# Kernel tuning notes

Hardware: AMD Instinct MI355X
Metric: run time of the kernel (lower is better)

Reference implementation:

```python
import jax, jax.numpy as jnp
import numpy as np

DIM = 1024
HEADS = 16
HEAD_DIM = DIM // HEADS
B, N = 8, 1024


def setup_inputs() -> dict:
    key = jax.random.key(0)
    ks = jax.random.split(key, 10)
    s = lambda fan_in: 1.0 / np.sqrt(fan_in)
    return {
        "x": jax.random.normal(ks[0], (B, N, DIM), jnp.float32),
        "pose_angles": jax.random.normal(ks[1], (B, 3), jnp.float32),
        # weights stored (in, out) so y = x @ W + b (equivalent to torch Linear)
        "Wqkv": jax.random.normal(ks[2], (DIM, 3 * DIM), jnp.float32) * s(DIM),
        "bqkv": jnp.zeros((3 * DIM,), jnp.float32),
        "W1": jax.random.normal(ks[3], (3, 64), jnp.float32) * s(3),
        "b1": jnp.zeros((64,), jnp.float32),
        "W2": jax.random.normal(ks[4], (64, 3 * DIM), jnp.float32) * s(64),
        "b2": jnp.zeros((3 * DIM,), jnp.float32),
        "Wproj": jax.random.normal(ks[5], (DIM, DIM), jnp.float32) * s(DIM),
        "bproj": jnp.zeros((DIM,), jnp.float32),
    }


def reference(x, pose_angles, Wqkv, bqkv, W1, b1, W2, b2, Wproj, bproj):
    Bq, Nq, C = x.shape
    H, D = HEADS, HEAD_DIM
    # qkv projection -> [B,N,3,H,D] -> [3,B,H,N,D]
    qkv = (x @ Wqkv + bqkv).reshape(Bq, Nq, 3, H, D).transpose(2, 0, 3, 1, 4)
    q, k, v = qkv[0], qkv[1], qkv[2]
    # pose MLP: 3 -> 64 -> 3*dim, chunked into per-head biases [B,H,1,D]
    pose_emb = jax.nn.relu(pose_angles @ W1 + b1) @ W2 + b2
    pose_q, pose_k, pose_v = jnp.split(pose_emb, 3, axis=1)
    pose_q = pose_q.reshape(Bq, H, 1, D)
    pose_k = pose_k.reshape(Bq, H, 1, D)
    pose_v = pose_v.reshape(Bq, H, 1, D)
    q = q + pose_q
    k = k + pose_k
    v = v + pose_v
    scale = 1.0 / jnp.sqrt(jnp.asarray(D, x.dtype))
    attn = jax.nn.softmax(jnp.einsum("bhnd,bhmd->bhnm", q, k) * scale, axis=-1)
    # dropout is identity in eval mode
    out = jnp.einsum("bhnm,bhmd->bhnd", attn, v)
    out = out.transpose(0, 2, 1, 3).reshape(Bq, Nq, C)
    return out @ Wproj + bproj
```

## Files before the change

### kernel.cpp

```cpp
#include <hip/hip_runtime.h>
#include <stdint.h>

typedef unsigned short u16;
typedef short bf16x8 __attribute__((ext_vector_type(8)));
typedef short bf16x4 __attribute__((ext_vector_type(4)));
typedef float f32x4 __attribute__((ext_vector_type(4)));
typedef u16 u16x4 __attribute__((ext_vector_type(4)));

__device__ __forceinline__ u16 f2bf(float f) {
  union { float f; unsigned int u; } v; v.f = f;
  unsigned int r = v.u + 0x7fffu + ((v.u >> 16) & 1u);
  return (u16)(r >> 16);
}

__device__ __forceinline__ void async16(const void* g, void* l) {
  __builtin_amdgcn_global_load_lds(
      (const __attribute__((address_space(1))) unsigned int*)g,
      (__attribute__((address_space(3))) unsigned int*)l, 16, 0, 0);
}

__device__ __forceinline__ f32x4 mfma16x16(bf16x4 a, bf16x4 b, f32x4 c) {
#if __has_builtin(__builtin_amdgcn_mfma_f32_16x16x16bf16_1k)
  return __builtin_amdgcn_mfma_f32_16x16x16bf16_1k(a, b, c, 0, 0, 0);
#else
  asm volatile("v_mfma_f32_16x16x16_bf16 %0, %1, %2, %0\n\ts_nop 7\n\ts_nop 7"
               : "+v"(c) : "v"(a), "v"(b));
  return c;
#endif
}

__global__ void pose_mlp_kernel(const float* __restrict__ ang, const float* __restrict__ W1,
                                const float* __restrict__ b1, const float* __restrict__ W2,
                                const float* __restrict__ b2, float* __restrict__ pose) {
  __shared__ float hid[8][64];
  int t = threadIdx.x;
  for (int idx = t; idx < 512; idx += 256) {
    int b = idx >> 6, j = idx & 63;
    float a = b1[j];
#pragma unroll
    for (int i = 0; i < 3; ++i) a += ang[b * 3 + i] * W1[i * 64 + j];
    hid[b][j] = fmaxf(a, 0.f);
  }
  __syncthreads();
  int idx = blockIdx.x * 256 + t;
  int b = idx / 3072, c = idx - b * 3072;
  float a = b2[c];
#pragma unroll
  for (int j = 0; j < 64; ++j) a += hid[b][j] * W2[j * 3072 + c];
  pose[idx] = a;
}

__global__ void cast_x_kernel(const float4* __restrict__ x, u16x4* __restrict__ y, int n4) {
  int i = blockIdx.x * blockDim.x + threadIdx.x;
  const int stride = gridDim.x * blockDim.x;
  for (; i < n4; i += stride) {
    float4 v = x[i];
    u16x4 o;
    o[0] = f2bf(v.x); o[1] = f2bf(v.y); o[2] = f2bf(v.z); o[3] = f2bf(v.w);
    y[i] = o;
  }
}

__global__ void transpose_cast_kernel(const float* __restrict__ W, u16* __restrict__ Wt,
                                      int Kdim, int Ncol) {
  __shared__ float tile[64][65];
  const int tx = threadIdx.x, ty = threadIdx.y;
  const int c0 = blockIdx.x * 64, k0 = blockIdx.y * 64;
#pragma unroll
  for (int rr = 0; rr < 16; ++rr) {
    int row = rr * 4 + ty;
    tile[row][tx] = W[(size_t)(k0 + row) * Ncol + c0 + tx];
  }
  __syncthreads();
#pragma unroll
  for (int rr = 0; rr < 16; ++rr) {
    int row = rr * 4 + ty;
    Wt[(size_t)(c0 + row) * Kdim + k0 + tx] = f2bf(tile[tx][row]);
  }
}

template <int EPI>
__global__ void __launch_bounds__(256) gemm_bt_kernel(
    const u16* __restrict__ A, const u16* __restrict__ Bt,
    const float* __restrict__ bias, const float* __restrict__ pose,
    u16* __restrict__ qout, u16* __restrict__ kout, u16* __restrict__ vtout,
    float* __restrict__ cout, int Kdim, int Ncols, int nTilesX) {
  __shared__ u16 ldsA[2][128 * 64];
  __shared__ u16 ldsB[2][128 * 64];
  const int t = threadIdx.x, l = t & 63, w = t >> 6;
  const int g = l >> 4, r16 = l & 15;
  const int wr = w >> 1, wc = w & 1;
  const int xk = r16 & 7;
  const int nwg = gridDim.x, cpx = nwg >> 3;
  const int swz = (blockIdx.x & 7) * cpx + (blockIdx.x >> 3);
  const int n0 = (swz % nTilesX) * 128, m0 = (swz / nTilesX) * 128;
  const u16* Ab = A + (size_t)m0 * Kdim;
  const u16* Bb = Bt + (size_t)n0 * Kdim;

  auto stage = [&](int buf, int kt) {
#pragma unroll
    for (int ii = 0; ii < 4; ++ii) {
      int idx = ii * 256 + t, row = idx >> 3;
      int seg = (idx & 7) ^ (row & 7);
      async16(Ab + (size_t)row * Kdim + kt + seg * 8, &ldsA[buf][(ii * 256 + w * 64) * 8]);
    }
#pragma unroll
    for (int ii = 0; ii < 4; ++ii) {
      int idx = ii * 256 + t, row = idx >> 3;
      int seg = (idx & 7) ^ (row & 7);
      async16(Bb + (size_t)row * Kdim + kt + seg * 8, &ldsB[buf][(ii * 256 + w * 64) * 8]);
    }
  };

  f32x4 acc[4][4] = {};
  const int nIter = Kdim >> 6;
  stage(0, 0);
  asm volatile("s_waitcnt vmcnt(0)" ::: "memory");
  __builtin_amdgcn_s_barrier();
  int cur = 0;
  for (int it = 0; it < nIter; ++it) {
    if (it + 1 < nIter) stage(cur ^ 1, (it + 1) << 6);
#pragma unroll
    for (int ks = 0; ks < 2; ++ks) {
      bf16x8 a[4], bb[4];
#pragma unroll
      for (int i = 0; i < 4; ++i)
        a[i] = *(const bf16x8*)&ldsA[cur][(wr * 64 + i * 16 + r16) * 64 + ((ks * 4 + g) ^ xk) * 8];
#pragma unroll
      for (int j = 0; j < 4; ++j)
        bb[j] = *(const bf16x8*)&ldsB[cur][(wc * 64 + j * 16 + r16) * 64 + ((ks * 4 + g) ^ xk) * 8];
#pragma unroll
      for (int i = 0; i < 4; ++i)
#pragma unroll
        for (int j = 0; j < 4; ++j)
          acc[i][j] = __builtin_amdgcn_mfma_f32_16x16x32_bf16(a[i], bb[j], acc[i][j], 0, 0, 0);
    }
    asm volatile("s_waitcnt vmcnt(0)" ::: "memory");
    __builtin_amdgcn_s_barrier();
    cur ^= 1;
  }
#pragma unroll
  for (int i = 0; i < 4; ++i)
#pragma unroll
    for (int j = 0; j < 4; ++j)
#pragma unroll
      for (int r = 0; r < 4; ++r) {
        int row = m0 + wr * 64 + i * 16 + g * 4 + r;
        int col = n0 + wc * 64 + j * 16 + r16;
        float v = acc[i][j][r] + bias[col];
        if (EPI == 0) {
          int b = row >> 10, n = row & 1023;
          v += pose[b * 3072 + col];
          u16 hv = f2bf(v);
          int three = col >> 10, hh = (col >> 6) & 15, d = col & 63;
          size_t bhh = (size_t)(b * 16 + hh);
          if (three == 0)      qout[(bhh * 1024 + n) * 64 + d] = hv;
          else if (three == 1) kout[(bhh * 1024 + n) * 64 + d] = hv;
          else                 vtout[(bhh * 64 + d) * 1024 + n] = hv;
        } else {
          cout[(size_t)row * Ncols + col] = v;
        }
      }
}

__global__ void __launch_bounds__(256) attn_kernel(
    const u16* __restrict__ Qb, const u16* __restrict__ Kb,
    const u16* __restrict__ Vtb, u16* __restrict__ aout) {
  __shared__ u16 ldsK[64][72];
  __shared__ u16 ldsV[64][72];
  const int t = threadIdx.x, l = t & 63, w = t >> 6;
  const int g = l >> 4, r16 = l & 15;
  const int bh = blockIdx.x >> 4, qt = blockIdx.x & 15;
  const int b = bh >> 4, h = bh & 15;
  const int q0 = qt * 64 + w * 16;
  const u16* Qp = Qb + ((size_t)bh * 1024 + q0 + r16) * 64;
  bf16x8 qreg0 = *(const bf16x8*)(Qp + g * 8);
  bf16x8 qreg1 = *(const bf16x8*)(Qp + 32 + g * 8);
  const u16* Kbase = Kb + (size_t)bh * 1024 * 64;
  const u16* Vbase = Vtb + (size_t)bh * 64 * 1024;
  float m = -1e30f, rs = 0.f;
  f32x4 o[4] = {};
  for (int key0 = 0; key0 < 1024; key0 += 64) {
#pragma unroll
    for (int ii = 0; ii < 2; ++ii) {
      int idx = ii * 256 + t, row = idx >> 3, seg = idx & 7;
      *(bf16x8*)&ldsK[row][seg * 8] = *(const bf16x8*)(Kbase + (size_t)(key0 + row) * 64 + seg * 8);
      *(bf16x8*)&ldsV[row][seg * 8] = *(const bf16x8*)(Vbase + (size_t)row * 1024 + key0 + seg * 8);
    }
    __syncthreads();
    f32x4 s[4] = {};
#pragma unroll
    for (int f = 0; f < 4; ++f) {
      bf16x8 ak0 = *(const bf16x8*)&ldsK[f * 16 + r16][g * 8];
      s[f] = __builtin_amdgcn_mfma_f32_16x16x32_bf16(ak0, qreg0, s[f], 0, 0, 0);
      bf16x8 ak1 = *(const bf16x8*)&ldsK[f * 16 + r16][32 + g * 8];
      s[f] = __builtin_amdgcn_mfma_f32_16x16x32_bf16(ak1, qreg1, s[f], 0, 0, 0);
    }
    float mt = -1e30f;
#pragma unroll
    for (int f = 0; f < 4; ++f)
#pragma unroll
      for (int r = 0; r < 4; ++r) { s[f][r] *= 0.125f; mt = fmaxf(mt, s[f][r]); }
    mt = fmaxf(mt, __shfl_xor(mt, 16));
    mt = fmaxf(mt, __shfl_xor(mt, 32));
    float mnew = fmaxf(m, mt);
    float alpha = __expf(m - mnew);
    float rt = 0.f;
    bf16x4 pa[4];
#pragma unroll
    for (int f = 0; f < 4; ++f) {
#pragma unroll
      for (int r = 0; r < 4; ++r) {
        float p = __expf(s[f][r] - mnew);
        rt += p;
        pa[f][r] = (short)f2bf(p);
      }
    }
    rt += __shfl_xor(rt, 16);
    rt += __shfl_xor(rt, 32);
    rs = rs * alpha + rt;
    m = mnew;
    float ar[4];
#pragma unroll
    for (int r = 0; r < 4; ++r) ar[r] = __shfl(alpha, (l & 48) | (g * 4 + r));
#pragma unroll
    for (int nf = 0; nf < 4; ++nf)
#pragma unroll
      for (int r = 0; r < 4; ++r) o[nf][r] *= ar[r];
#pragma unroll
    for (int s4 = 0; s4 < 4; ++s4)
#pragma unroll
      for (int nf = 0; nf < 4; ++nf) {
        bf16x4 bv = *(const bf16x4*)&ldsV[nf * 16 + r16][s4 * 16 + g * 4];
        o[nf] = mfma16x16(pa[s4], bv, o[nf]);
      }
    __syncthreads();
  }
  float rr[4];
#pragma unroll
  for (int r = 0; r < 4; ++r) rr[r] = __shfl(1.0f / rs, (l & 48) | (g * 4 + r));
#pragma unroll
  for (int nf = 0; nf < 4; ++nf)
#pragma unroll
    for (int r = 0; r < 4; ++r) {
      int qq = qt * 64 + w * 16 + g * 4 + r;
      int d = nf * 16 + r16;
      aout[((size_t)b * 1024 + qq) * 1024 + h * 64 + d] = f2bf(o[nf][r] * rr[r]);
    }
}

extern "C" void kernel_launch(void* const* d_in, const int* in_sizes, int n_in,
                              void* d_out, int out_size, void* d_ws, size_t ws_size,
                              hipStream_t stream) {
  (void)in_sizes; (void)n_in; (void)out_size; (void)ws_size;
  const float* x     = (const float*)d_in[0];
  const float* ang   = (const float*)d_in[1];
  const float* Wqkv  = (const float*)d_in[2];
  const float* bqkv  = (const float*)d_in[3];
  const float* W1    = (const float*)d_in[4];
  const float* b1    = (const float*)d_in[5];
  const float* W2    = (const float*)d_in[6];
  const float* b2    = (const float*)d_in[7];
  const float* Wproj = (const float*)d_in[8];
  const float* bproj = (const float*)d_in[9];
  float* out = (float*)d_out;
  char* ws = (char*)d_ws;

  u16* xh     = (u16*)(ws);
  u16* wqkvt  = (u16*)(ws + (size_t)16 * 1024 * 1024);
  u16* wprojt = (u16*)(ws + (size_t)22 * 1024 * 1024);
  float* pose = (float*)(ws + (size_t)24 * 1024 * 1024);
  u16* Qb     = (u16*)(ws + (size_t)25 * 1024 * 1024);
  u16* Kb     = (u16*)(ws + (size_t)41 * 1024 * 1024);
  u16* Vtb    = (u16*)(ws + (size_t)57 * 1024 * 1024);

  pose_mlp_kernel<<<96, 256, 0, stream>>>(ang, W1, b1, W2, b2, pose);
  cast_x_kernel<<<2048, 256, 0, stream>>>((const float4*)x, (u16x4*)xh, 8 * 1024 * 1024 / 4);
  transpose_cast_kernel<<<dim3(48, 16), dim3(64, 4), 0, stream>>>(Wqkv, wqkvt, 1024, 3072);
  transpose_cast_kernel<<<dim3(16, 16), dim3(64, 4), 0, stream>>>(Wproj, wprojt, 1024, 1024);
  gemm_bt_kernel<0><<<1536, 256, 0, stream>>>(xh, wqkvt, bqkv, pose,
                                              Qb, Kb, Vtb, nullptr, 1024, 3072, 24);
  attn_kernel<<<2048, 256, 0, stream>>>(Qb, Kb, Vtb, xh);
  gemm_bt_kernel<1><<<512, 256, 0, stream>>>(xh, wprojt, bproj, nullptr,
                                             nullptr, nullptr, nullptr, out, 1024, 1024, 8);
}
```

Baseline: 217.1 us.

## Replace 128x128 GEMM with 8-wave 256-row tile and phased prefetch

The GEMM kernel is rewritten to use 512 threads (8 waves) and 256-row M tiles, with N tiles of 256 for the QKV projection and 128 for the output projection. The next K-tile's global-to-LDS loads are split into stages spread across four compute phases, and MFMA sections are wrapped in s_setprio for overlap. Larger tiles cut global traffic per FLOP, and interleaving loads with compute aims to hide memory latency. In exchange the kernel uses more LDS and registers per block, and the grids shrink to 384 and 256 blocks, which may underfill the GPU's CUs.

```diff
diff --git a/kernel.cpp b/kernel.cpp
--- a/kernel.cpp
+++ b/kernel.cpp
@@ -79,75 +79,107 @@
   }
 }
 
-template <int EPI>
-__global__ void __launch_bounds__(256) gemm_bt_kernel(
+template <int EPI, int NJF>
+__global__ void __launch_bounds__(512) gemm8_kernel(
     const u16* __restrict__ A, const u16* __restrict__ Bt,
     const float* __restrict__ bias, const float* __restrict__ pose,
     u16* __restrict__ qout, u16* __restrict__ kout, u16* __restrict__ vtout,
     float* __restrict__ cout, int Kdim, int Ncols, int nTilesX) {
-  __shared__ u16 ldsA[2][128 * 64];
-  __shared__ u16 ldsB[2][128 * 64];
+  constexpr int BN = NJF * 64;
+  constexpr int NJH = NJF / 2;
+  constexpr int NST = 2 + NJF / 2;
+  constexpr int BOFF = 256 * 64;
+  __shared__ u16 lds[2][(256 + BN) * 64];
   const int t = threadIdx.x, l = t & 63, w = t >> 6;
   const int g = l >> 4, r16 = l & 15;
-  const int wr = w >> 1, wc = w & 1;
+  const int wr = w >> 2, wc = w & 3;
   const int xk = r16 & 7;
   const int nwg = gridDim.x, cpx = nwg >> 3;
   const int swz = (blockIdx.x & 7) * cpx + (blockIdx.x >> 3);
-  const int n0 = (swz % nTilesX) * 128, m0 = (swz / nTilesX) * 128;
+  const int n0 = (swz % nTilesX) * BN, m0 = (swz / nTilesX) * 256;
   const u16* Ab = A + (size_t)m0 * Kdim;
   const u16* Bb = Bt + (size_t)n0 * Kdim;
 
-  auto stage = [&](int buf, int kt) {
-#pragma unroll
-    for (int ii = 0; ii < 4; ++ii) {
-      int idx = ii * 256 + t, row = idx >> 3;
+  auto stage = [&](int buf, int kt, int st) {
+#pragma unroll
+    for (int it = 0; it < 2; ++it) {
+      int idx = it * 512 + t;
+      int row = idx >> 3;
       int seg = (idx & 7) ^ (row & 7);
-      async16(Ab + (size_t)row * Kdim + kt + seg * 8, &ldsA[buf][(ii * 256 + w * 64) * 8]);
-    }
-#pragma unroll
-    for (int ii = 0; ii < 4; ++ii) {
-      int idx = ii * 256 + t, row = idx >> 3;
-      int seg = (idx & 7) ^ (row & 7);
-      async16(Bb + (size_t)row * Kdim + kt + seg * 8, &ldsB[buf][(ii * 256 + w * 64) * 8]);
+      if (st < 2) {
+        async16(Ab + (size_t)(st * 128 + row) * Kdim + kt + seg * 8,
+                &lds[buf][st * 128 * 64 + idx * 8]);
+      } else {
+        async16(Bb + (size_t)((st - 2) * 128 + row) * Kdim + kt + seg * 8,
+                &lds[buf][BOFF + (st - 2) * 128 * 64 + idx * 8]);
+      }
     }
   };
 
-  f32x4 acc[4][4] = {};
-  const int nIter = Kdim >> 6;
-  stage(0, 0);
-  asm volatile("s_waitcnt vmcnt(0)" ::: "memory");
-  __builtin_amdgcn_s_barrier();
-  int cur = 0;
-  for (int it = 0; it < nIter; ++it) {
-    if (it + 1 < nIter) stage(cur ^ 1, (it + 1) << 6);
-#pragma unroll
-    for (int ks = 0; ks < 2; ++ks) {
-      bf16x8 a[4], bb[4];
-#pragma unroll
-      for (int i = 0; i < 4; ++i)
-        a[i] = *(const bf16x8*)&ldsA[cur][(wr * 64 + i * 16 + r16) * 64 + ((ks * 4 + g) ^ xk) * 8];
-#pragma unroll
-      for (int j = 0; j < 4; ++j)
-        bb[j] = *(const bf16x8*)&ldsB[cur][(wc * 64 + j * 16 + r16) * 64 + ((ks * 4 + g) ^ xk) * 8];
-#pragma unroll
-      for (int i = 0; i < 4; ++i)
-#pragma unroll
-        for (int j = 0; j < 4; ++j)
-          acc[i][j] = __builtin_amdgcn_mfma_f32_16x16x32_bf16(a[i], bb[j], acc[i][j], 0, 0, 0);
-    }
-    asm volatile("s_waitcnt vmcnt(0)" ::: "memory");
-    __builtin_amdgcn_s_barrier();
-    cur ^= 1;
-  }
-#pragma unroll
-  for (int i = 0; i < 4; ++i)
-#pragma unroll
-    for (int j = 0; j < 4; ++j)
+  f32x4 acc[8][NJF] = {};
+  const int nT = Kdim >> 6;
+#pragma unroll
+  for (int st = 0; st < NST; ++st) stage(0, 0, st);
+
+  for (int tt = 0; tt < nT; ++tt) {
+    const int cur = tt & 1, nxt = cur ^ 1;
+    const bool pf = (tt + 1 < nT);
+    const int ktn = (tt + 1) << 6;
+#pragma unroll
+    for (int ph = 0; ph < 4; ++ph) {
+      const int mh = ph >> 1, nh = ph & 1;
+      if (ph == 0) {
+        if (pf) {
+          stage(nxt, ktn, 0);
+          __builtin_amdgcn_sched_barrier(0);
+          asm volatile("s_waitcnt vmcnt(2)" ::: "memory");
+        } else {
+          asm volatile("s_waitcnt vmcnt(0)" ::: "memory");
+        }
+        __builtin_amdgcn_s_barrier();
+        __builtin_amdgcn_sched_barrier(0);
+      } else {
+        if (pf && ph < NST) stage(nxt, ktn, ph);
+      }
+      bf16x8 af[4][2], bfr[NJH][2];
+#pragma unroll
+      for (int mi2 = 0; mi2 < 4; ++mi2)
+#pragma unroll
+        for (int ks = 0; ks < 2; ++ks) {
+          int arow = wr * 128 + (mh * 4 + mi2) * 16 + r16;
+          af[mi2][ks] = *(const bf16x8*)&lds[cur][arow * 64 + (((ks * 4 + g) ^ xk)) * 8];
+        }
+#pragma unroll
+      for (int nj2 = 0; nj2 < NJH; ++nj2)
+#pragma unroll
+        for (int ks = 0; ks < 2; ++ks) {
+          int brow = wc * (NJF * 16) + (nh * NJH + nj2) * 16 + r16;
+          bfr[nj2][ks] = *(const bf16x8*)&lds[cur][BOFF + brow * 64 + (((ks * 4 + g) ^ xk)) * 8];
+        }
+      if (ph != 0) __builtin_amdgcn_s_barrier();
+      __builtin_amdgcn_s_setprio(1);
+#pragma unroll
+      for (int ks = 0; ks < 2; ++ks)
+#pragma unroll
+        for (int mi2 = 0; mi2 < 4; ++mi2)
+#pragma unroll
+          for (int nj2 = 0; nj2 < NJH; ++nj2)
+            acc[mh * 4 + mi2][nh * NJH + nj2] = __builtin_amdgcn_mfma_f32_16x16x32_bf16(
+                af[mi2][ks], bfr[nj2][ks], acc[mh * 4 + mi2][nh * NJH + nj2], 0, 0, 0);
+      __builtin_amdgcn_s_setprio(0);
+      __builtin_amdgcn_s_barrier();
+    }
+  }
+
+#pragma unroll
+  for (int mi = 0; mi < 8; ++mi)
+#pragma unroll
+    for (int nj = 0; nj < NJF; ++nj)
 #pragma unroll
       for (int r = 0; r < 4; ++r) {
-        int row = m0 + wr * 64 + i * 16 + g * 4 + r;
-        int col = n0 + wc * 64 + j * 16 + r16;
-        float v = acc[i][j][r] + bias[col];
+        int row = m0 + wr * 128 + mi * 16 + g * 4 + r;
+        int col = n0 + wc * (NJF * 16) + nj * 16 + r16;
+        float v = acc[mi][nj][r] + bias[col];
         if (EPI == 0) {
           int b = row >> 10, n = row & 1023;
           v += pose[b * 3072 + col];
@@ -278,9 +310,9 @@
   cast_x_kernel<<<2048, 256, 0, stream>>>((const float4*)x, (u16x4*)xh, 8 * 1024 * 1024 / 4);
   transpose_cast_kernel<<<dim3(48, 16), dim3(64, 4), 0, stream>>>(Wqkv, wqkvt, 1024, 3072);
   transpose_cast_kernel<<<dim3(16, 16), dim3(64, 4), 0, stream>>>(Wproj, wprojt, 1024, 1024);
-  gemm_bt_kernel<0><<<1536, 256, 0, stream>>>(xh, wqkvt, bqkv, pose,
-                                              Qb, Kb, Vtb, nullptr, 1024, 3072, 24);
+  gemm8_kernel<0, 4><<<384, 512, 0, stream>>>(xh, wqkvt, bqkv, pose,
+                                              Qb, Kb, Vtb, nullptr, 1024, 3072, 12);
   attn_kernel<<<2048, 256, 0, stream>>>(Qb, Kb, Vtb, xh);
-  gemm_bt_kernel<1><<<512, 256, 0, stream>>>(xh, wprojt, bproj, nullptr,
-                                             nullptr, nullptr, nullptr, out, 1024, 1024, 8);
-}
+  gemm8_kernel<1, 2><<<256, 512, 0, stream>>>(xh, wprojt, bproj, nullptr,
+                                              nullptr, nullptr, nullptr, out, 1024, 1024, 8);
+}
```

Result: slower. 234.6 us (+8.1%).

## Replace GEMM with 256x256-tile 8-wave eight-phase pipelined kernel

Applied to the files above, without the earlier changes.

Both projection GEMMs now use 256x256 output tiles with 512 threads (8 waves). Loads are staged in 128-row quarter-tiles across two LDS slots, and an eight-phase schedule interleaves async global->LDS loads, LDS fragment reads and MFMA bursts under s_setprio, using fine-grained waitcnt and barriers. The goal is more reuse per tile and hiding of memory latency behind MFMA. In exchange it uses large LDS (128KB) and heavy register pressure, and the output projection launches only 128 blocks, which may underfill the GPU.

```diff
diff --git a/kernel.cpp b/kernel.cpp
--- a/kernel.cpp
+++ b/kernel.cpp
@@ -80,74 +80,138 @@
 }
 
 template <int EPI>
-__global__ void __launch_bounds__(256) gemm_bt_kernel(
+__global__ void __launch_bounds__(512, 2) gemm_8ph_kernel(
     const u16* __restrict__ A, const u16* __restrict__ Bt,
     const float* __restrict__ bias, const float* __restrict__ pose,
     u16* __restrict__ qout, u16* __restrict__ kout, u16* __restrict__ vtout,
     float* __restrict__ cout, int Kdim, int Ncols, int nTilesX) {
-  __shared__ u16 ldsA[2][128 * 64];
-  __shared__ u16 ldsB[2][128 * 64];
+  constexpr int BREG = 256 * 64;
+  constexpr int SLOT = 512 * 64;
+  __shared__ u16 lds[2][SLOT];
   const int t = threadIdx.x, l = t & 63, w = t >> 6;
   const int g = l >> 4, r16 = l & 15;
-  const int wr = w >> 1, wc = w & 1;
+  const int wr = w >> 2, wc = w & 3;
   const int xk = r16 & 7;
   const int nwg = gridDim.x, cpx = nwg >> 3;
   const int swz = (blockIdx.x & 7) * cpx + (blockIdx.x >> 3);
-  const int n0 = (swz % nTilesX) * 128, m0 = (swz / nTilesX) * 128;
+  const int n0 = (swz % nTilesX) * 256, m0 = (swz / nTilesX) * 256;
   const u16* Ab = A + (size_t)m0 * Kdim;
   const u16* Bb = Bt + (size_t)n0 * Kdim;
 
-  auto stage = [&](int buf, int kt) {
-#pragma unroll
-    for (int ii = 0; ii < 4; ++ii) {
-      int idx = ii * 256 + t, row = idx >> 3;
+  auto stage = [&](int slot, int hr, int kt) {
+#pragma unroll
+    for (int it = 0; it < 2; ++it) {
+      int idx = it * 512 + t, row = idx >> 3;
       int seg = (idx & 7) ^ (row & 7);
-      async16(Ab + (size_t)row * Kdim + kt + seg * 8, &ldsA[buf][(ii * 256 + w * 64) * 8]);
-    }
-#pragma unroll
-    for (int ii = 0; ii < 4; ++ii) {
-      int idx = ii * 256 + t, row = idx >> 3;
-      int seg = (idx & 7) ^ (row & 7);
-      async16(Bb + (size_t)row * Kdim + kt + seg * 8, &ldsB[buf][(ii * 256 + w * 64) * 8]);
-    }
-  };
-
-  f32x4 acc[4][4] = {};
-  const int nIter = Kdim >> 6;
-  stage(0, 0);
-  asm volatile("s_waitcnt vmcnt(0)" ::: "memory");
-  __builtin_amdgcn_s_barrier();
-  int cur = 0;
-  for (int it = 0; it < nIter; ++it) {
-    if (it + 1 < nIter) stage(cur ^ 1, (it + 1) << 6);
-#pragma unroll
-    for (int ks = 0; ks < 2; ++ks) {
-      bf16x8 a[4], bb[4];
-#pragma unroll
-      for (int i = 0; i < 4; ++i)
-        a[i] = *(const bf16x8*)&ldsA[cur][(wr * 64 + i * 16 + r16) * 64 + ((ks * 4 + g) ^ xk) * 8];
-#pragma unroll
-      for (int j = 0; j < 4; ++j)
-        bb[j] = *(const bf16x8*)&ldsB[cur][(wc * 64 + j * 16 + r16) * 64 + ((ks * 4 + g) ^ xk) * 8];
-#pragma unroll
-      for (int i = 0; i < 4; ++i)
-#pragma unroll
-        for (int j = 0; j < 4; ++j)
-          acc[i][j] = __builtin_amdgcn_mfma_f32_16x16x32_bf16(a[i], bb[j], acc[i][j], 0, 0, 0);
-    }
-    asm volatile("s_waitcnt vmcnt(0)" ::: "memory");
+      const u16* src = (hr < 2) ? Ab + (size_t)(hr * 128 + row) * Kdim + kt + seg * 8
+                                : Bb + (size_t)((hr - 2) * 128 + row) * Kdim + kt + seg * 8;
+      int dst = ((hr < 2) ? hr * 128 * 64 : BREG + (hr - 2) * 128 * 64) + idx * 8;
+      async16(src, &lds[slot][dst]);
+    }
+  };
+
+  f32x4 acc[8][4] = {};
+  bf16x8 aF[4][2], bF0[2][2], bF1[2][2];
+
+  auto readA = [&](int slot, int mh) {
+#pragma unroll
+    for (int mi2 = 0; mi2 < 4; ++mi2)
+#pragma unroll
+      for (int ks = 0; ks < 2; ++ks)
+        aF[mi2][ks] = *(const bf16x8*)&lds[slot][(mh * 128 + wr * 64 + mi2 * 16 + r16) * 64 +
+                                                ((ks * 4 + g) ^ xk) * 8];
+  };
+  auto readB = [&](int slot, int nh, bf16x8 (&bF)[2][2]) {
+#pragma unroll
+    for (int nj2 = 0; nj2 < 2; ++nj2)
+#pragma unroll
+      for (int ks = 0; ks < 2; ++ks)
+        bF[nj2][ks] = *(const bf16x8*)&lds[slot][BREG + (nh * 128 + wc * 32 + nj2 * 16 + r16) * 64 +
+                                                ((ks * 4 + g) ^ xk) * 8];
+  };
+  auto bar = [&]() {
+    asm volatile("" ::: "memory");
     __builtin_amdgcn_s_barrier();
-    cur ^= 1;
-  }
-#pragma unroll
-  for (int i = 0; i < 4; ++i)
-#pragma unroll
-    for (int j = 0; j < 4; ++j)
+    asm volatile("" ::: "memory");
+  };
+  auto lgk = [&]() {
+    asm volatile("s_waitcnt lgkmcnt(0)" ::: "memory");
+    __builtin_amdgcn_sched_barrier(0);
+  };
+  auto mmac = [&](int mh, int nh, bf16x8 (&bF)[2][2]) {
+    __builtin_amdgcn_s_setprio(1);
+#pragma unroll
+    for (int ks = 0; ks < 2; ++ks)
+#pragma unroll
+      for (int mi2 = 0; mi2 < 4; ++mi2)
+#pragma unroll
+        for (int nj2 = 0; nj2 < 2; ++nj2)
+          acc[mh * 4 + mi2][nh * 2 + nj2] = __builtin_amdgcn_mfma_f32_16x16x32_bf16(
+              aF[mi2][ks], bF[nj2][ks], acc[mh * 4 + mi2][nh * 2 + nj2], 0, 0, 0);
+    __builtin_amdgcn_s_setprio(0);
+  };
+
+  const int nIter = Kdim >> 7;
+  stage(0, 0, 0); stage(0, 2, 0); stage(0, 3, 0); stage(0, 1, 0);
+  stage(1, 0, 64); stage(1, 2, 64);
+
+  for (int i = 0; i < nIter; ++i) {
+    const bool pf = (i + 1 < nIter);
+    const int k1 = (2 * i + 1) << 6, k2 = (2 * i + 2) << 6, k3 = (2 * i + 3) << 6;
+    stage(1, 3, k1);
+    __builtin_amdgcn_sched_barrier(0);
+    asm volatile("s_waitcnt vmcnt(6)" ::: "memory");
+    bar();
+    readA(0, 0); readB(0, 0, bF0);
+    lgk();
+    mmac(0, 0, bF0);
+    stage(1, 1, k1);
+    bar();
+    readB(0, 1, bF1);
+    lgk();
+    mmac(0, 1, bF1);
+    if (pf) stage(0, 0, k2);
+    bar();
+    readA(0, 1);
+    lgk();
+    mmac(1, 0, bF0);
+    if (pf) stage(0, 2, k2);
+    bar();
+    lgk();
+    mmac(1, 1, bF1);
+    if (pf) stage(0, 3, k2);
+    __builtin_amdgcn_sched_barrier(0);
+    if (pf) asm volatile("s_waitcnt vmcnt(6)" ::: "memory");
+    else    asm volatile("s_waitcnt vmcnt(0)" ::: "memory");
+    bar();
+    readA(1, 0); readB(1, 0, bF0);
+    lgk();
+    mmac(0, 0, bF0);
+    if (pf) stage(0, 1, k2);
+    bar();
+    readB(1, 1, bF1);
+    lgk();
+    mmac(0, 1, bF1);
+    if (pf) stage(1, 0, k3);
+    bar();
+    readA(1, 1);
+    lgk();
+    mmac(1, 0, bF0);
+    if (pf) stage(1, 2, k3);
+    bar();
+    lgk();
+    mmac(1, 1, bF1);
+  }
+
+#pragma unroll
+  for (int mi = 0; mi < 8; ++mi)
+#pragma unroll
+    for (int nj = 0; nj < 4; ++nj)
 #pragma unroll
       for (int r = 0; r < 4; ++r) {
-        int row = m0 + wr * 64 + i * 16 + g * 4 + r;
-        int col = n0 + wc * 64 + j * 16 + r16;
-        float v = acc[i][j][r] + bias[col];
+        int row = m0 + (mi >> 2) * 128 + wr * 64 + (mi & 3) * 16 + g * 4 + r;
+        int col = n0 + (nj >> 1) * 128 + wc * 32 + (nj & 1) * 16 + r16;
+        float v = acc[mi][nj][r] + bias[col];
         if (EPI == 0) {
           int b = row >> 10, n = row & 1023;
           v += pose[b * 3072 + col];
@@ -278,9 +342,9 @@
   cast_x_kernel<<<2048, 256, 0, stream>>>((const float4*)x, (u16x4*)xh, 8 * 1024 * 1024 / 4);
   transpose_cast_kernel<<<dim3(48, 16), dim3(64, 4), 0, stream>>>(Wqkv, wqkvt, 1024, 3072);
   transpose_cast_kernel<<<dim3(16, 16), dim3(64, 4), 0, stream>>>(Wproj, wprojt, 1024, 1024);
-  gemm_bt_kernel<0><<<1536, 256, 0, stream>>>(xh, wqkvt, bqkv, pose,
-                                              Qb, Kb, Vtb, nullptr, 1024, 3072, 24);
+  gemm_8ph_kernel<0><<<384, 512, 0, stream>>>(xh, wqkvt, bqkv, pose,
+                                              Qb, Kb, Vtb, nullptr, 1024, 3072, 12);
   attn_kernel<<<2048, 256, 0, stream>>>(Qb, Kb, Vtb, xh);
-  gemm_bt_kernel<1><<<512, 256, 0, stream>>>(xh, wprojt, bproj, nullptr,
-                                             nullptr, nullptr, nullptr, out, 1024, 1024, 8);
-}
+  gemm_8ph_kernel<1><<<128, 512, 0, stream>>>(xh, wprojt, bproj, nullptr,
+                                              nullptr, nullptr, nullptr, out, 1024, 1024, 4);
+}
```

Result: slower. 221.9 us (+2.2%).
